# Kernel optimization log

Hardware: AMD Instinct MI355X
Metric: run time of the kernel (lower is better)

## Reference

```python
import jax, jax.numpy as jnp
import numpy as np

NUM_TAGS = 256
BATCH = 64
SEQ = 1024


def setup_inputs() -> dict:
    key = jax.random.key(0)
    k1, k2, k3, k4, k5 = jax.random.split(key, 5)
    emissions = jax.random.normal(k1, (BATCH, SEQ, NUM_TAGS), dtype=jnp.float32)
    tags = jax.random.randint(k2, (BATCH, SEQ), 0, NUM_TAGS, dtype=jnp.int64)
    mask = jnp.ones((BATCH, SEQ), dtype=bool)
    # params mimic nn.init.uniform_(-0.1, 0.1)
    transitions = jax.random.uniform(k3, (NUM_TAGS, NUM_TAGS), jnp.float32, -0.1, 0.1)
    start_transitions = jax.random.uniform(k4, (NUM_TAGS,), jnp.float32, -0.1, 0.1)
    end_transitions = jax.random.uniform(k5, (NUM_TAGS,), jnp.float32, -0.1, 0.1)
    return {
        "emissions": emissions,
        "transitions": transitions,
        "start_transitions": start_transitions,
        "end_transitions": end_transitions,
        "tags": tags,
        "mask": mask,
    }


def _compute_normalizer(emissions, mask, transitions, start_transitions, end_transitions):
    # emissions: [B,S,T], mask: [B,S] bool
    score0 = start_transitions[None, :] + emissions[:, 0]  # [B,T]

    def step(score, xs):
        em_i, m_i = xs  # em_i: [B,T], m_i: [B]
        # [B, prev, next]
        next_score = jax.nn.logsumexp(
            score[:, :, None] + transitions[None, :, :] + em_i[:, None, :], axis=1
        )
        score = jnp.where(m_i[:, None], next_score, score)
        return score, None

    em_rest = jnp.swapaxes(emissions[:, 1:], 0, 1)  # [S-1,B,T]
    mk_rest = jnp.swapaxes(mask[:, 1:], 0, 1)       # [S-1,B]
    score, _ = jax.lax.scan(step, score0, (em_rest, mk_rest))
    return jax.nn.logsumexp(score + end_transitions[None, :], axis=1)  # [B]


def _compute_score(emissions, tags, mask, transitions, start_transitions, end_transitions):
    # gather emission score of the gold tag at each position: [B,S]
    em_g = jnp.take_along_axis(emissions, tags[:, :, None], axis=2)[:, :, 0]
    # transitions indexed [cur_tag, prev_tag] to match the torch code exactly
    trans_g = transitions[tags[:, 1:], tags[:, :-1]]  # [B,S-1]
    mf = mask[:, 1:].astype(emissions.dtype)
    score = start_transitions[tags[:, 0]] + em_g[:, 0]
    score = score + jnp.sum((trans_g + em_g[:, 1:]) * mf, axis=1)
    seq_ends = mask.astype(jnp.int32).sum(axis=1) - 1  # [B]
    last_tags = jnp.take_along_axis(tags, seq_ends[:, None].astype(tags.dtype), axis=1)[:, 0]
    return score + end_transitions[last_tags]


def reference(emissions, transitions, start_transitions, end_transitions, tags, mask):
    nll = _compute_normalizer(emissions, mask, transitions, start_transitions, end_transitions) \
        - _compute_score(emissions, tags, mask, transitions, start_transitions, end_transitions)
    return jnp.mean(nll)  # reduction='mean'
```

## Files before the change

### kernel.cpp

```cpp
#include <hip/hip_runtime.h>
#include <math.h>

#define NTAGS 256
#define BATCH 64
#define SEQ   1024
#define BPB   16
#define NBLK  (BATCH / BPB)

typedef float f32x4 __attribute__((ext_vector_type(4)));
typedef short bf16x8 __attribute__((ext_vector_type(8)));

__device__ __forceinline__ unsigned short rne_bf16(float x) {
    unsigned u = __float_as_uint(x);
    return (unsigned short)((u + 0x7FFFu + ((u >> 16) & 1u)) >> 16);
}
__device__ __forceinline__ unsigned cvt_pk_bf16(float lo, float hi) {
    unsigned r;
    asm("v_cvt_pk_bf16_f32 %0, %1, %2" : "=v"(r) : "v"(lo), "v"(hi));
    return r;
}
__device__ __forceinline__ void lds_barrier() {
    asm volatile("s_waitcnt lgkmcnt(0)\n\ts_barrier" ::: "memory");
}

__global__ __launch_bounds__(512)
void crf_normalizer_kernel(
    const float* __restrict__ em,
    const float* __restrict__ trans,
    const float* __restrict__ startT,
    const float* __restrict__ endT,
    float* __restrict__ norm_out)
{
    const int tid = threadIdx.x;
    const int w   = tid >> 6;
    const int l   = tid & 63;
    const int l15 = l & 15;
    const int hi  = (l >> 4) & 3;
    const int bb0 = blockIdx.x * BPB;

    __shared__ __align__(16) unsigned short Vb[2][BPB * NTAGS];
    __shared__ __align__(16) float Rld[2][BPB];
    __shared__ __align__(16) float P2[BPB][BPB];

    bf16x8 Af[2][8];
#pragma unroll
    for (int mt = 0; mt < 2; ++mt) {
        const int j = ((w << 1) + mt) * 16 + l15;
#pragma unroll
        for (int kk = 0; kk < 8; ++kk) {
            bf16x8 v;
#pragma unroll
            for (int e = 0; e < 8; ++e)
                v[e] = (short)rne_bf16(__expf(trans[(kk * 32 + hi * 8 + e) * NTAGS + j]));
            Af[mt][kk] = v;
        }
    }

    if (tid < 256) {
        const int b  = tid & 15;
        const int jg = tid >> 4;
        const float* e0 = em + (size_t)(bb0 + b) * SEQ * NTAGS + jg * 16;
        float vals[16];
#pragma unroll
        for (int q = 0; q < 4; ++q) {
            f32x4 ev = *reinterpret_cast<const f32x4*>(&e0[q * 4]);
            f32x4 sv = *reinterpret_cast<const f32x4*>(&startT[jg * 16 + q * 4]);
#pragma unroll
            for (int c = 0; c < 4; ++c)
                vals[q * 4 + c] = __expf(ev[c] + sv[c]);
        }
#pragma unroll
        for (int half = 0; half < 2; ++half) {
            unsigned pk[4];
#pragma unroll
            for (int q = 0; q < 4; ++q)
                pk[q] = cvt_pk_bf16(vals[half * 8 + 2 * q], vals[half * 8 + 2 * q + 1]);
            const int byte = b * 512 + ((jg * 32 + half * 16) ^ (b << 4));
            *reinterpret_cast<uint4*>(reinterpret_cast<char*>(&Vb[0][0]) + byte) =
                *reinterpret_cast<const uint4*>(pk);
        }
        if (jg == 0)
            Rld[0][b] = __expf(-(startT[0] + em[(size_t)(bb0 + b) * SEQ * NTAGS]));
    }

    int boffh[8];
#pragma unroll
    for (int kk = 0; kk < 8; ++kk)
        boffh[kk] = (l15 * 512 + ((kk * 64 + hi * 16) ^ (l15 << 4))) >> 1;
    int woff[2];
#pragma unroll
    for (int mt = 0; mt < 2; ++mt) {
        const int gmt = (w << 1) + mt;
        woff[mt] = l15 * 512 + ((gmt * 32 + hi * 8) ^ (l15 << 4));
    }

    const float* emP = em + ((size_t)(bb0 + l15) * SEQ + 1) * NTAGS + (w << 5) + (hi << 2);
    f32x4 emA0 = *reinterpret_cast<const f32x4*>(emP);
    f32x4 emA1 = *reinterpret_cast<const f32x4*>(emP + 16);
    f32x4 emB0 = *reinterpret_cast<const f32x4*>(emP + NTAGS);
    f32x4 emB1 = *reinterpret_cast<const f32x4*>(emP + NTAGS + 16);

    double S = 0.0;
    __syncthreads();

#define CRF_STEP(PR, EM0, EM1, DOPREF)                                        \
    do {                                                                      \
        const float q_ = Rld[(PR)][l15];                \
        bf16x8 Bf0[4];                                                        \
        _Pragma("unroll")                                                     \
        for (int kk = 0; kk < 4; ++kk)                                        \
            Bf0[kk] = *reinterpret_cast<const bf16x8*>(&Vb[(PR)][boffh[kk]]); \
        f32x4 xf0, xf1;                                                       \
        xf0[0] = __expf(EM0[0]); xf0[1] = __expf(EM0[1]);                     \
        xf0[2] = __expf(EM0[2]); xf0[3] = __expf(EM0[3]);                     \
        xf1[0] = __expf(EM1[0]); xf1[1] = __expf(EM1[1]);                     \
        xf1[2] = __expf(EM1[2]); xf1[3] = __expf(EM1[3]);                     \
        if (DOPREF) {     \
            EM0 = *reinterpret_cast<const f32x4*>(emP + 2 * NTAGS);           \
            EM1 = *reinterpret_cast<const f32x4*>(emP + 2 * NTAGS + 16);      \
        }                                                                     \
        emP += NTAGS;                                                         \
        f32x4 ac0 = {0,0,0,0}, ac1 = {0,0,0,0};                               \
        _Pragma("unroll")                                                     \
        for (int kk = 0; kk < 4; ++kk) {                                      \
            ac0 = __builtin_amdgcn_mfma_f32_16x16x32_bf16(Af[0][kk], Bf0[kk], ac0, 0, 0, 0); \
            ac1 = __builtin_amdgcn_mfma_f32_16x16x32_bf16(Af[1][kk], Bf0[kk], ac1, 0, 0, 0); \
        }                                                                     \
        bf16x8 Bf1[4];                                                        \
        _Pragma("unroll")                                                     \
        for (int kk = 0; kk < 4; ++kk)                                        \
            Bf1[kk] = *reinterpret_cast<const bf16x8*>(&Vb[(PR)][boffh[kk + 4]]); \
        _Pragma("unroll")                                                     \
        for (int kk = 0; kk < 4; ++kk) {                                      \
            ac0 = __builtin_amdgcn_mfma_f32_16x16x32_bf16(Af[0][kk + 4], Bf1[kk], ac0, 0, 0, 0); \
            ac1 = __builtin_amdgcn_mfma_f32_16x16x32_bf16(Af[1][kk + 4], Bf1[kk], ac1, 0, 0, 0); \
        }                                                                     \
        const f32x4 cf0 = xf0 * q_;                                           \
        const f32x4 cf1 = xf1 * q_;                                           \
        const f32x4 sv0 = ac0 * cf0;                                          \
        const f32x4 sv1 = ac1 * cf1;                                          \
        char* const wbase = reinterpret_cast<char*>(&Vb[1 - (PR)][0]);        \
        uint2 p0, p1;                                                         \
        p0.x = cvt_pk_bf16(sv0[0], sv0[1]); p0.y = cvt_pk_bf16(sv0[2], sv0[3]); \
        p1.x = cvt_pk_bf16(sv1[0], sv1[1]); p1.y = cvt_pk_bf16(sv1[2], sv1[3]); \
        *reinterpret_cast<uint2*>(wbase + woff[0]) = p0;                      \
        *reinterpret_cast<uint2*>(wbase + woff[1]) = p1;                      \
        if (tid < 16) {                                                       \
            S -= (double)__logf(q_);                                          \
            Rld[1 - (PR)][l15] = __builtin_amdgcn_rcpf(ac0[0] * cf0[0]);      \
        }                                                                     \
        lds_barrier();                                                        \
    } while (0)

    for (int u = 0; u < 510; ++u) {
        CRF_STEP(0, emA0, emA1, 1);
        CRF_STEP(1, emB0, emB1, 1);
    }
    CRF_STEP(0, emA0, emA1, 1);
    CRF_STEP(1, emB0, emB1, 0);
    CRF_STEP(0, emA0, emA1, 0);
#undef CRF_STEP

    __syncthreads();

    if (tid < 256) {
        const int b  = tid & 15;
        const int jg = tid >> 4;
        float accv = 0.f;
#pragma unroll
        for (int half = 0; half < 2; ++half) {
            const int byte = b * 512 + ((jg * 32 + half * 16) ^ (b << 4));
            bf16x8 vv = *reinterpret_cast<const bf16x8*>(
                reinterpret_cast<const char*>(&Vb[1][0]) + byte);
#pragma unroll
            for (int e = 0; e < 8; ++e) {
                const float f = __uint_as_float(((unsigned)(unsigned short)vv[e]) << 16);
                accv += f * __expf(endT[jg * 16 + half * 8 + e]);
            }
        }
        P2[b][jg] = accv;
    }
    __syncthreads();
    if (tid < 16) {
        float tot = 0.f;
#pragma unroll
        for (int g = 0; g < 16; ++g) tot += P2[tid][g];
        norm_out[bb0 + tid] = (float)(S + (double)__logf(tot));
    }
}

__global__ __launch_bounds__(256) void crf_score_kernel(
    const float* __restrict__ em,
    const float* __restrict__ trans,
    const float* __restrict__ startT,
    const float* __restrict__ endT,
    const int* __restrict__ tags,
    float* __restrict__ score_out)
{
    const int b   = blockIdx.x;
    const int tid = threadIdx.x;
    const int* tg = tags + b * SEQ;
    const float* emb = em + (size_t)b * SEQ * NTAGS;

    float s = 0.f;
    for (int t = tid; t < SEQ; t += 256) {
        int cur = tg[t];
        float v = emb[t * NTAGS + cur];
        v += (t == 0) ? startT[cur] : trans[cur * NTAGS + tg[t - 1]];
        s += v;
    }
    __shared__ float red[4];
#pragma unroll
    for (int off = 32; off > 0; off >>= 1)
        s += __shfl_xor(s, off);
    if ((tid & 63) == 0) red[tid >> 6] = s;
    __syncthreads();
    if (tid == 0)
        score_out[b] = red[0] + red[1] + red[2] + red[3] + endT[tg[SEQ - 1]];
}

__global__ void crf_finalize_kernel(const float* __restrict__ norm,
                                    const float* __restrict__ score,
                                    float* __restrict__ out)
{
    const int tid = threadIdx.x;
    float v = norm[tid] - score[tid];
#pragma unroll
    for (int off = 32; off > 0; off >>= 1)
        v += __shfl_xor(v, off);
    if (tid == 0) out[0] = v * (1.0f / BATCH);
}

extern "C" void kernel_launch(void* const* d_in, const int* in_sizes, int n_in,
                              void* d_out, int out_size, void* d_ws, size_t ws_size,
                              hipStream_t stream)
{
    const float* em     = (const float*)d_in[0];
    const float* trans  = (const float*)d_in[1];
    const float* startT = (const float*)d_in[2];
    const float* endT   = (const float*)d_in[3];
    const int*   tags   = (const int*)d_in[4];

    float* ws    = (float*)d_ws;
    float* norm  = ws;
    float* score = ws + BATCH;

    crf_normalizer_kernel<<<NBLK, 512, 0, stream>>>(em, trans, startT, endT, norm);
    crf_score_kernel<<<BATCH, 256, 0, stream>>>(em, trans, startT, endT, tags, score);
    crf_finalize_kernel<<<1, 64, 0, stream>>>(norm, score, (float*)d_out);
}
```

Measured before the change: 462.6 us.

## Precompute exp(emissions) in parallel pre-pass and split MFMA accumulator chains

Adds a fully parallel kernel that writes exp(emissions) to workspace, so the latency-bound sequential normalizer loop only loads ready-made exponentials instead of running eight expf per step. Each MFMA accumulation chain is split into two independent accumulators that are summed afterwards, which shortens the dependency chain. The MFMA section is also wrapped in s_setprio to raise wave priority. The cost is an extra 64 MB read and 64 MB write pass, plus a dependence on workspace size; without enough workspace the old path runs.

Result: slower. 542.2 us (+17.2%).

```diff
diff --git a/kernel.cpp b/kernel.cpp
--- a/kernel.cpp
+++ b/kernel.cpp
@@ -23,9 +23,26 @@
     asm volatile("s_waitcnt lgkmcnt(0)\n\ts_barrier" ::: "memory");
 }
 
+__global__ __launch_bounds__(256) void crf_expem_kernel(
+    const float* __restrict__ em, float* __restrict__ X)
+{
+    const size_t n4 = (size_t)BATCH * SEQ * NTAGS / 4;
+    const size_t stride = (size_t)gridDim.x * blockDim.x;
+    const float4* in  = (const float4*)em;
+    float4*       out = (float4*)X;
+    for (size_t i = (size_t)blockIdx.x * blockDim.x + threadIdx.x; i < n4; i += stride) {
+        float4 v = in[i];
+        v.x = __expf(v.x); v.y = __expf(v.y);
+        v.z = __expf(v.z); v.w = __expf(v.w);
+        out[i] = v;
+    }
+}
+
+template<int USEX>
 __global__ __launch_bounds__(512)
 void crf_normalizer_kernel(
     const float* __restrict__ em,
+    const float* __restrict__ emsrc,
     const float* __restrict__ trans,
     const float* __restrict__ startT,
     const float* __restrict__ endT,
@@ -94,7 +111,7 @@
         woff[mt] = l15 * 512 + ((gmt * 32 + hi * 8) ^ (l15 << 4));
     }
 
-    const float* emP = em + ((size_t)(bb0 + l15) * SEQ + 1) * NTAGS + (w << 5) + (hi << 2);
+    const float* emP = emsrc + ((size_t)(bb0 + l15) * SEQ + 1) * NTAGS + (w << 5) + (hi << 2);
     f32x4 emA0 = *reinterpret_cast<const f32x4*>(emP);
     f32x4 emA1 = *reinterpret_cast<const f32x4*>(emP + 16);
     f32x4 emB0 = *reinterpret_cast<const f32x4*>(emP + NTAGS);
@@ -111,30 +128,39 @@
         for (int kk = 0; kk < 4; ++kk)                                        \
             Bf0[kk] = *reinterpret_cast<const bf16x8*>(&Vb[(PR)][boffh[kk]]); \
         f32x4 xf0, xf1;                                                       \
-        xf0[0] = __expf(EM0[0]); xf0[1] = __expf(EM0[1]);                     \
-        xf0[2] = __expf(EM0[2]); xf0[3] = __expf(EM0[3]);                     \
-        xf1[0] = __expf(EM1[0]); xf1[1] = __expf(EM1[1]);                     \
-        xf1[2] = __expf(EM1[2]); xf1[3] = __expf(EM1[3]);                     \
-        if (DOPREF) {     \
+        if (USEX) {                                                           \
+            xf0 = EM0; xf1 = EM1;              \
+        } else {                                                              \
+            xf0[0] = __expf(EM0[0]); xf0[1] = __expf(EM0[1]);                 \
+            xf0[2] = __expf(EM0[2]); xf0[3] = __expf(EM0[3]);                 \
+            xf1[0] = __expf(EM1[0]); xf1[1] = __expf(EM1[1]);                 \
+            xf1[2] = __expf(EM1[2]); xf1[3] = __expf(EM1[3]);                 \
+        }                                                                     \
+        if (DOPREF) {       \
             EM0 = *reinterpret_cast<const f32x4*>(emP + 2 * NTAGS);           \
             EM1 = *reinterpret_cast<const f32x4*>(emP + 2 * NTAGS + 16);      \
         }                                                                     \
         emP += NTAGS;                                                         \
-        f32x4 ac0 = {0,0,0,0}, ac1 = {0,0,0,0};                               \
-        _Pragma("unroll")                                                     \
-        for (int kk = 0; kk < 4; ++kk) {                                      \
-            ac0 = __builtin_amdgcn_mfma_f32_16x16x32_bf16(Af[0][kk], Bf0[kk], ac0, 0, 0, 0); \
-            ac1 = __builtin_amdgcn_mfma_f32_16x16x32_bf16(Af[1][kk], Bf0[kk], ac1, 0, 0, 0); \
+        f32x4 a0 = {0,0,0,0}, a1 = {0,0,0,0};                                 \
+        f32x4 b0 = {0,0,0,0}, b1 = {0,0,0,0};                                 \
+        __builtin_amdgcn_s_setprio(1);                                        \
+        _Pragma("unroll")                                                     \
+        for (int kk = 0; kk < 4; ++kk) {            \
+            a0 = __builtin_amdgcn_mfma_f32_16x16x32_bf16(Af[0][kk], Bf0[kk], a0, 0, 0, 0); \
+            a1 = __builtin_amdgcn_mfma_f32_16x16x32_bf16(Af[1][kk], Bf0[kk], a1, 0, 0, 0); \
         }                                                                     \
         bf16x8 Bf1[4];                                                        \
         _Pragma("unroll")                                                     \
         for (int kk = 0; kk < 4; ++kk)                                        \
             Bf1[kk] = *reinterpret_cast<const bf16x8*>(&Vb[(PR)][boffh[kk + 4]]); \
         _Pragma("unroll")                                                     \
-        for (int kk = 0; kk < 4; ++kk) {                                      \
-            ac0 = __builtin_amdgcn_mfma_f32_16x16x32_bf16(Af[0][kk + 4], Bf1[kk], ac0, 0, 0, 0); \
-            ac1 = __builtin_amdgcn_mfma_f32_16x16x32_bf16(Af[1][kk + 4], Bf1[kk], ac1, 0, 0, 0); \
-        }                                                                     \
+        for (int kk = 0; kk < 4; ++kk) {           \
+            b0 = __builtin_amdgcn_mfma_f32_16x16x32_bf16(Af[0][kk + 4], Bf1[kk], b0, 0, 0, 0); \
+            b1 = __builtin_amdgcn_mfma_f32_16x16x32_bf16(Af[1][kk + 4], Bf1[kk], b1, 0, 0, 0); \
+        }                                                                     \
+        __builtin_amdgcn_s_setprio(0);                                        \
+        const f32x4 ac0 = a0 + b0;                                            \
+        const f32x4 ac1 = a1 + b1;                                            \
         const f32x4 cf0 = xf0 * q_;                                           \
         const f32x4 cf1 = xf1 * q_;                                           \
         const f32x4 sv0 = ac0 * cf0;                                          \
@@ -245,7 +271,17 @@
     float* norm  = ws;
     float* score = ws + BATCH;
 
-    crf_normalizer_kernel<<<NBLK, 512, 0, stream>>>(em, trans, startT, endT, norm);
+    const size_t xoff   = 512;
+    const size_t xbytes = (size_t)BATCH * SEQ * NTAGS * sizeof(float);
+    float* X = (float*)((char*)d_ws + xoff);
+    const bool usex = (ws_size >= xoff + xbytes);
+
+    if (usex) {
+        crf_expem_kernel<<<2048, 256, 0, stream>>>(em, X);
+        crf_normalizer_kernel<1><<<NBLK, 512, 0, stream>>>(em, X, trans, startT, endT, norm);
+    } else {
+        crf_normalizer_kernel<0><<<NBLK, 512, 0, stream>>>(em, em, trans, startT, endT, norm);
+    }
     crf_score_kernel<<<BATCH, 256, 0, stream>>>(em, trans, startT, endT, tags, score);
     crf_finalize_kernel<<<1, 64, 0, stream>>>(norm, score, (float*)d_out);
 }
```
